# Kernel tuning notes

Measured on AMD Instinct MI355X. Metric: run time of the kernel, lower is better.

The kernel has to match this reference:

```python
import jax, jax.numpy as jnp
import numpy as np

DIM = 384
HEADS = 12
HEAD_DIM = DIM // HEADS
WS = 7          # window_size
SS = 3          # shift_size (SW-MSA)
DIM_FF = 4 * DIM
EPS = 1e-5


def _rel_pos_index():
    coords = np.stack(np.meshgrid(np.arange(WS), np.arange(WS), indexing='ij'))
    cf = coords.reshape(2, -1)                       # (2, 49)
    rel = cf[:, :, None] - cf[:, None, :]            # (2, 49, 49)
    rel = rel.transpose(1, 2, 0).astype(np.int64)
    rel[:, :, 0] += WS - 1
    rel[:, :, 1] += WS - 1
    rel[:, :, 0] *= 2 * WS - 1
    return rel.sum(-1)                               # (49, 49)


def _attn_mask(Hp, Wp):
    # cyclic-shift mask, computed on static shapes with numpy
    img = np.zeros((Hp, Wp))
    slices = (slice(0, -WS), slice(-WS, -SS), slice(-SS, None))
    cnt = 0
    for hs in slices:
        for ws_ in slices:
            img[hs, ws_] = cnt
            cnt += 1
    mw = img.reshape(Hp // WS, WS, Wp // WS, WS).transpose(0, 2, 1, 3).reshape(-1, WS * WS)
    am = mw[:, None, :] - mw[:, :, None]             # unsqueeze(1) - unsqueeze(2)
    am = np.where(am != 0, -100.0, 0.0)
    return jnp.asarray(am, jnp.float32)              # (nW, 49, 49)


def _ln(x, g, b):
    mu = jnp.mean(x, -1, keepdims=True)
    var = jnp.mean(jnp.square(x - mu), -1, keepdims=True)
    return (x - mu) * jax.lax.rsqrt(var + EPS) * g + b


def setup_inputs() -> dict:
    key = jax.random.key(0)
    ks = jax.random.split(key, 8)
    B, H, W = 32, 56, 56
    s = 0.02
    return {
        'x': jax.random.normal(ks[0], (B, H * W, DIM), jnp.float32),
        'H': H, 'W': W,
        'rel_idx': jnp.asarray(_rel_pos_index(), jnp.int32),
        'rpb_table': jax.random.normal(ks[1], ((2 * WS - 1) ** 2, HEADS), jnp.float32) * s,
        'qkv_w': jax.random.normal(ks[2], (DIM, 3 * DIM), jnp.float32) * s,
        'proj_w': jax.random.normal(ks[3], (DIM, DIM), jnp.float32) * s,
        'proj_b': jnp.zeros((DIM,), jnp.float32),
        'norm1_g': jnp.ones((DIM,), jnp.float32),
        'norm1_b': jnp.zeros((DIM,), jnp.float32),
        'norm2_g': jnp.ones((DIM,), jnp.float32),
        'norm2_b': jnp.zeros((DIM,), jnp.float32),
        'ffn_w1': jax.random.normal(ks[4], (DIM, DIM_FF), jnp.float32) * s,
        'ffn_b1': jnp.zeros((DIM_FF,), jnp.float32),
        'ffn_w2': jax.random.normal(ks[5], (DIM_FF, DIM), jnp.float32) * s,
        'ffn_b2': jnp.zeros((DIM,), jnp.float32),
    }


def reference(x, H, W, rel_idx, rpb_table, qkv_w, proj_w, proj_b,
              norm1_g, norm1_b, norm2_g, norm2_b,
              ffn_w1, ffn_b1, ffn_w2, ffn_b2):
    B, L, C = x.shape
    shortcut = x
    h = _ln(x, norm1_g, norm1_b).reshape(B, H, W, C)

    pad_b = (WS - H % WS) % WS
    pad_r = (WS - W % WS) % WS
    if pad_b > 0 or pad_r > 0:
        h = jnp.pad(h, ((0, 0), (0, pad_b), (0, pad_r), (0, 0)))
    Hp, Wp = H + pad_b, W + pad_r

    if SS > 0:
        h = jnp.roll(h, (-SS, -SS), axis=(1, 2))

    # window partition -> (B*nW, 49, C)
    nHw, nWw = Hp // WS, Wp // WS
    win = h.reshape(B, nHw, WS, nWw, WS, C).transpose(0, 1, 3, 2, 4, 5)
    win = win.reshape(-1, WS * WS, C)
    Bw, N = win.shape[0], WS * WS

    # window attention
    qkv = (win @ qkv_w).reshape(Bw, N, 3, HEADS, HEAD_DIM)
    q, k, v = [qkv[:, :, i].transpose(0, 2, 1, 3) for i in range(3)]  # (Bw, heads, N, hd)
    attn = jnp.einsum('bhnd,bhmd->bhnm', q, k) / np.sqrt(HEAD_DIM)

    bias = rpb_table[rel_idx]                      # (N, N, heads)
    attn = attn + bias.transpose(2, 0, 1)[None]

    if SS > 0:
        mask = _attn_mask(Hp, Wp)                  # (nW, N, N)
        nW = mask.shape[0]
        attn = attn.reshape(B, nW, HEADS, N, N) + mask[None, :, None]
        attn = attn.reshape(Bw, HEADS, N, N)

    attn = jax.nn.softmax(attn, axis=-1)
    out = jnp.einsum('bhnm,bhmd->bnhd', attn, v).reshape(Bw, N, C)
    out = out @ proj_w + proj_b

    # window reverse
    out = out.reshape(B, nHw, nWw, WS, WS, C).transpose(0, 1, 3, 2, 4, 5)
    out = out.reshape(B, Hp, Wp, C)
    if SS > 0:
        out = jnp.roll(out, (SS, SS), axis=(1, 2))
    if pad_b > 0 or pad_r > 0:
        out = out[:, :H, :W, :]

    h = shortcut + out.reshape(B, H * W, C)
    ff = _ln(h, norm2_g, norm2_b)
    ff = jax.nn.gelu(ff @ ffn_w1 + ffn_b1, approximate=False) @ ffn_w2 + ffn_b2
    return h + ff
```

## Files before the change

### kernel.cpp

```cpp
#include <hip/hip_runtime.h>

#define DEV __device__ __forceinline__

typedef __bf16 bf16x8 __attribute__((ext_vector_type(8)));
typedef float  f32x4  __attribute__((ext_vector_type(4)));
typedef unsigned short u16x8 __attribute__((ext_vector_type(8)));
typedef unsigned short u16x4 __attribute__((ext_vector_type(4)));
typedef long  longx2 __attribute__((ext_vector_type(2)));

DEV float b2f(unsigned short u) {
    unsigned int t = ((unsigned int)u) << 16;
    return __uint_as_float(t);
}
DEV unsigned short f2b(float f) {
    unsigned int u = __float_as_uint(f);
    unsigned int r = (u + 0x7FFFu + ((u >> 16) & 1u)) >> 16;
    return (unsigned short)r;
}
DEV unsigned char f2f8(float f) {
    return (unsigned char)(__builtin_amdgcn_cvt_pk_fp8_f32(f, f, 0, false) & 0xff);
}

DEV int kpos(int c) {
    int s = (c >> 3) & 7;
    return (c & ~63) | ((((s & 3) << 1) | (s >> 2)) << 3) | (c & 7);
}

DEV void gload_lds16(const void* g, void* l) {
    __builtin_amdgcn_global_load_lds(
        (const __attribute__((address_space(1))) void*)g,
        (__attribute__((address_space(3))) void*)l, 16, 0, 0);
}

DEV size_t win_to_tok(int row) {
    int w = row / 49, t = row - w * 49;
    int b  = w >> 6, widx = w & 63;
    int wi = widx >> 3, wj = widx & 7;
    int ti = t / 7, tj = t - ti * 7;
    int hh = wi * 7 + ti + 3; if (hh >= 56) hh -= 56;
    int ww = wj * 7 + tj + 3; if (ww >= 56) ww -= 56;
    return (size_t)b * 3136 + (size_t)hh * 56 + ww;
}

__global__ void wprep8(const float* __restrict__ src, unsigned char* __restrict__ dst,
                       int K, int N) {
    int idx = blockIdx.x * 256 + threadIdx.x;
    if (idx >= K * N) return;
    int k = idx / N, n = idx - k * N;
    dst[(size_t)n * K + kpos(k)] = f2f8(src[idx]);
}

__global__ void btab_build(const int* __restrict__ rel_idx, const float* __restrict__ rpb,
                           float* __restrict__ tab) {
    int idx = blockIdx.x * 256 + threadIdx.x;
    if (idx >= 4 * 12 * 64 * 64) return;
    int col = idx & 63, row = (idx >> 6) & 63;
    int h = (idx >> 12) % 12, cls = idx / (12 * 4096);
    float v;
    if (row >= 49 || col >= 49) {
        v = -10000.f;
    } else {
        v = rpb[rel_idx[row * 49 + col] * 12 + h];
        int ti = row / 7, tj = row - (row / 7) * 7;
        int si = col / 7, sj = col - (col / 7) * 7;
        int lq = ((cls & 2) ? (ti < 4 ? 1 : 2) : 0) * 3 + ((cls & 1) ? (tj < 4 ? 1 : 2) : 0);
        int lk = ((cls & 2) ? (si < 4 ? 1 : 2) : 0) * 3 + ((cls & 1) ? (sj < 4 ? 1 : 2) : 0);
        if (lq != lk) v -= 100.f;
    }
    tab[idx] = v;
}

template <int REMAP>
__global__ __launch_bounds__(256) void ln_kernel(const float* __restrict__ x,
                                                 const float* __restrict__ g,
                                                 const float* __restrict__ b,
                                                 unsigned char* __restrict__ out,
                                                 int rows) {
    int r = blockIdx.x * 4 + (threadIdx.x >> 6);
    int lane = threadIdx.x & 63;
    if (r >= rows) return;
    size_t src = REMAP ? win_to_tok(r) : (size_t)r;
    const float* xp = x + src * 384;
    float v[6];
    float s = 0.f;
#pragma unroll
    for (int i = 0; i < 6; ++i) { v[i] = xp[i * 64 + lane]; s += v[i]; }
#pragma unroll
    for (int off = 32; off; off >>= 1) s += __shfl_xor(s, off, 64);
    float mu = s * (1.f / 384.f);
    float q = 0.f;
#pragma unroll
    for (int i = 0; i < 6; ++i) { float d = v[i] - mu; q += d * d; }
#pragma unroll
    for (int off = 32; off; off >>= 1) q += __shfl_xor(q, off, 64);
    float inv = rsqrtf(q * (1.f / 384.f) + 1e-5f);
    unsigned char* op = out + (size_t)r * 384;
#pragma unroll
    for (int i = 0; i < 6; ++i) {
        int c = i * 64 + lane;
        op[kpos(c)] = f2f8((v[i] - mu) * inv * g[c] + b[c]);
    }
}

template <int MODE, int NBUF, int DEPTH, int SB, int MINW>
__global__ __launch_bounds__(256, MINW) void gemm_f8_kernel(const unsigned char* __restrict__ A,
                                                            const unsigned char* __restrict__ Bt,
                                                            int M, int N, int K,
                                                            const float* __restrict__ bias,
                                                            const float* __restrict__ resid,
                                                            unsigned char* __restrict__ outb8,
                                                            unsigned short* __restrict__ outb,
                                                            float* __restrict__ outf) {
    static_assert(SB ? (NBUF >= DEPTH + 2) : (NBUF >= DEPTH + 1), "ring too small");
    __shared__ unsigned char As[NBUF][128 * 64];
    __shared__ unsigned char Bs[NBUF][128 * 64];
    const int tid = threadIdx.x;
    const int wid = tid >> 6, lane = tid & 63;
    const int ntile = N >> 7;

    int bid = blockIdx.x;
    int nwg = gridDim.x;
    int swb = ((nwg & 7) == 0) ? ((bid & 7) * (nwg >> 3) + (bid >> 3)) : bid;
    const int mt = swb / ntile, nt = swb - mt * ntile;
    const int wr = wid >> 1, wc = wid & 1;

    f32x4 acc[4][4] = {};

    const unsigned char* Abase = A  + (size_t)(mt * 128) * K;
    const unsigned char* Bbase = Bt + (size_t)(nt * 128) * K;

    auto stage = [&](int buf, int k0) {
#pragma unroll
        for (int j = 0; j < 2; ++j) {
            int r  = j * 64 + (tid >> 2);
            int gp = (tid & 3) ^ ((r >> 1) & 3);
            gload_lds16(Abase + (size_t)r * K + k0 + gp * 16, &As[buf][j * 4096 + tid * 16]);
            gload_lds16(Bbase + (size_t)r * K + k0 + gp * 16, &Bs[buf][j * 4096 + tid * 16]);
        }
    };

    const int fr = lane & 15, kq = lane >> 4;
    const int rowA = wr * 64 + fr;
    const int rowB = wc * 64 + fr;
    const int cb = (kq ^ ((fr >> 1) & 3)) << 4;

    const int nk = K >> 6;
    stage(0, 0);
    if (DEPTH >= 2 && nk > 1) stage(1, 64);

    for (int t = 0; t < nk; ++t) {
        const int cur = t % NBUF;
        if (t + DEPTH < nk) {
            stage((t + DEPTH) % NBUF, (t + DEPTH) << 6);
            if constexpr (DEPTH == 1) {
                asm volatile("s_waitcnt vmcnt(4)" ::: "memory");
            } else {
                asm volatile("s_waitcnt vmcnt(8)" ::: "memory");
            }
        } else if (DEPTH >= 2 && t + 1 < nk) {
            asm volatile("s_waitcnt vmcnt(4)" ::: "memory");
        } else {
            asm volatile("s_waitcnt vmcnt(0)" ::: "memory");
        }
        __builtin_amdgcn_s_barrier();

        longx2 a[4], b[4];
#pragma unroll
        for (int m = 0; m < 4; ++m)
            a[m] = *(const longx2*)(&As[cur][(rowA + m * 16) * 64 + cb]);
#pragma unroll
        for (int n = 0; n < 4; ++n)
            b[n] = *(const longx2*)(&Bs[cur][(rowB + n * 16) * 64 + cb]);
#pragma unroll
        for (int ks = 0; ks < 2; ++ks)
#pragma unroll
            for (int m = 0; m < 4; ++m)
#pragma unroll
                for (int n = 0; n < 4; ++n)
                    acc[m][n] = __builtin_amdgcn_mfma_f32_16x16x32_fp8_fp8(b[n][ks], a[m][ks], acc[m][n], 0, 0, 0);

        asm volatile("s_waitcnt lgkmcnt(0)" ::: "memory");
        if constexpr (SB == 0) __builtin_amdgcn_s_barrier();
    }

    const int row0 = mt * 128 + wr * 64;
    const int col0 = nt * 128 + wc * 64;
    const int rl = lane & 15;
    const int cq = (lane >> 4) << 2;
#pragma unroll
    for (int m = 0; m < 4; ++m) {
        int row = row0 + m * 16 + rl;
        size_t tok = 0;
        if constexpr (MODE == 1) tok = win_to_tok(row);
#pragma unroll
        for (int n = 0; n < 4; ++n) {
            int col = col0 + n * 16 + cq;
            f32x4 v = acc[m][n];
            if constexpr (MODE == 0) {
                u16x4 pk;
#pragma unroll
                for (int r = 0; r < 4; ++r) pk[r] = f2b(v[r]);
                *(u16x4*)&outb[(size_t)row * N + col] = pk;
            } else if constexpr (MODE == 1) {
                size_t o = tok * 384 + col;
                f32x4 rv = *(const f32x4*)&resid[o];
                f32x4 bb = *(const f32x4*)&bias[col];
                f32x4 ov = rv + v + bb;
                *(f32x4*)&outf[o] = ov;
            } else if constexpr (MODE == 2) {
                f32x4 bb = *(const f32x4*)&bias[col];
                float g4[4];
#pragma unroll
                for (int r = 0; r < 4; ++r) {
                    float t2 = v[r] + bb[r];
                    g4[r] = t2 / (1.f + __expf(-1.702f * t2));
                }
                int pk = 0;
                pk = __builtin_amdgcn_cvt_pk_fp8_f32(g4[0], g4[1], pk, false);
                pk = __builtin_amdgcn_cvt_pk_fp8_f32(g4[2], g4[3], pk, true);
                *(int*)(outb8 + (size_t)row * N + kpos(col)) = pk;
            } else {
                size_t o = (size_t)row * N + col;
                f32x4 rv = *(const f32x4*)&resid[o];
                f32x4 bb = *(const f32x4*)&bias[col];
                f32x4 ov = rv + v + bb;
                *(f32x4*)&outf[o] = ov;
            }
        }
    }
}

__global__ __launch_bounds__(256, 2) void attn_kernel(const unsigned short* __restrict__ QKV,
                                                      const float* __restrict__ Btab,
                                                      unsigned char* __restrict__ O8) {
    __shared__ char lds[65536];
    char* Kl = lds;
    char* Vl = lds + 16384;
    char* Pl = lds + 32768;

    const int w   = blockIdx.x;
    const int tid = threadIdx.x, wid = tid >> 6, lane = tid & 63;
    const int fr  = lane & 15, kq = lane >> 4;
    const size_t base = (size_t)w * 49 * 1152;
    const int widx = w & 63, wi = widx >> 3, wj = widx & 7;
    const int cls = ((wi == 7) ? 2 : 0) | ((wj == 7) ? 1 : 0);
    const float* tb = Btab + (size_t)cls * 12 * 4096;
    constexpr float SCL = 0.17677669529663687f;

    for (int R = 0; R < 3; ++R) {
        if (R) __syncthreads();
        {
            f32x4 z = {};
#pragma unroll
            for (int j = 0; j < 8; ++j) *(f32x4*)(lds + j * 4096 + tid * 16) = z;
        }
        __syncthreads();
        {
            int hh = tid >> 6, h = R * 4 + hh;
#pragma unroll
            for (int it = 0; it < 4; ++it) {
                int i = (tid & 63) + it * 64;
                if (i < 196) {
                    int m = i >> 2, c = i & 3;
                    u16x8 kv = *(const u16x8*)&QKV[base + (size_t)m * 1152 + 384 + h * 32 + c * 8];
                    *(u16x8*)(Kl + hh * 4096 + m * 64 + (c ^ ((m >> 1) & 3)) * 16) = kv;
                    u16x8 vv = *(const u16x8*)&QKV[base + (size_t)m * 1152 + 768 + h * 32 + c * 8];
#pragma unroll
                    for (int j = 0; j < 8; ++j) {
                        int d = c * 8 + j;
                        *(unsigned short*)(Vl + hh * 4096 + d * 128 +
                                           (((m >> 3) ^ (d & 7)) * 16) + (m & 7) * 2) = vv[j];
                    }
                }
            }
        }
        __syncthreads();

        const int h = R * 4 + wid;
        const float* tbh = tb + h * 4096;

        bf16x8 aq[4], bk[4];
#pragma unroll
        for (int mi = 0; mi < 4; ++mi) {
            int row = mi * 16 + fr; if (row > 48) row = 48;
            aq[mi] = *(const bf16x8*)&QKV[base + (size_t)row * 1152 + h * 32 + kq * 8];
        }
#pragma unroll
        for (int ni = 0; ni < 4; ++ni) {
            int rk = ni * 16 + fr;
            bk[ni] = *(const bf16x8*)(Kl + wid * 4096 + rk * 64 + ((kq ^ ((rk >> 1) & 3)) * 16));
        }
        f32x4 s[4][4] = {};
#pragma unroll
        for (int mi = 0; mi < 4; ++mi)
#pragma unroll
            for (int ni = 0; ni < 4; ++ni)
                s[mi][ni] = __builtin_amdgcn_mfma_f32_16x16x32_bf16(bk[ni], aq[mi], s[mi][ni], 0, 0, 0);

        float linv_[4];
#pragma unroll
        for (int mi = 0; mi < 4; ++mi) {
            int row = mi * 16 + fr;
            const float* tr = tbh + row * 64 + kq * 4;
            f32x4 sv[4];
            float mx = -1e30f;
#pragma unroll
            for (int ni = 0; ni < 4; ++ni) {
                f32x4 bb = *(const f32x4*)&tr[ni * 16];
                sv[ni] = s[mi][ni] * SCL + bb;
                mx = fmaxf(mx, fmaxf(fmaxf(sv[ni][0], sv[ni][1]), fmaxf(sv[ni][2], sv[ni][3])));
            }
            mx = fmaxf(mx, __shfl_xor(mx, 16, 64));
            mx = fmaxf(mx, __shfl_xor(mx, 32, 64));
            float sm = 0.f;
#pragma unroll
            for (int ni = 0; ni < 4; ++ni)
#pragma unroll
                for (int r = 0; r < 4; ++r) { sv[ni][r] = __expf(sv[ni][r] - mx); sm += sv[ni][r]; }
            sm += __shfl_xor(sm, 16, 64);
            sm += __shfl_xor(sm, 32, 64);
            linv_[mi] = 1.f / sm;
#pragma unroll
            for (int ni = 0; ni < 4; ++ni) {
                int colb = ni * 16 + kq * 4;
                int phys = (colb >> 3) ^ (row & 7);
                u16x4 pk;
#pragma unroll
                for (int r = 0; r < 4; ++r) pk[r] = f2b(sv[ni][r]);
                *(u16x4*)(Pl + wid * 8192 + row * 128 + phys * 16 + (colb & 7) * 2) = pk;
            }
        }
        asm volatile("s_waitcnt lgkmcnt(0)" ::: "memory");
        __builtin_amdgcn_sched_barrier(0);

        f32x4 oacc[4][2] = {};
#pragma unroll
        for (int sl = 0; sl < 2; ++sl) {
            bf16x8 bv[2];
#pragma unroll
            for (int ni = 0; ni < 2; ++ni) {
                int d = ni * 16 + fr;
                bv[ni] = *(const bf16x8*)(Vl + wid * 4096 + d * 128 + (((sl * 4 + kq) ^ (d & 7)) * 16));
            }
#pragma unroll
            for (int mi = 0; mi < 4; ++mi) {
                int row = mi * 16 + fr;
                bf16x8 ap = *(const bf16x8*)(Pl + wid * 8192 + row * 128 + (((sl * 4 + kq) ^ (row & 7)) * 16));
#pragma unroll
                for (int ni = 0; ni < 2; ++ni)
                    oacc[mi][ni] = __builtin_amdgcn_mfma_f32_16x16x32_bf16(bv[ni], ap, oacc[mi][ni], 0, 0, 0);
            }
        }

#pragma unroll
        for (int mi = 0; mi < 4; ++mi) {
            int row = mi * 16 + fr;
            if (row < 49) {
                float li = linv_[mi];
                unsigned char* opb = O8 + (size_t)(w * 49 + row) * 384;
#pragma unroll
                for (int ni = 0; ni < 2; ++ni) {
                    int c = h * 32 + ni * 16 + kq * 4;
                    int pk = 0;
                    pk = __builtin_amdgcn_cvt_pk_fp8_f32(oacc[mi][ni][0] * li, oacc[mi][ni][1] * li, pk, false);
                    pk = __builtin_amdgcn_cvt_pk_fp8_f32(oacc[mi][ni][2] * li, oacc[mi][ni][3] * li, pk, true);
                    *(int*)(opb + kpos(c)) = pk;
                }
            }
        }
    }
}

extern "C" void kernel_launch(void* const* d_in, const int* in_sizes, int n_in,
                              void* d_out, int out_size, void* d_ws, size_t ws_size,
                              hipStream_t stream) {
    const float* x     = (const float*)d_in[0];
    const int*   rel   = (const int*)  d_in[3];
    const float* rpb   = (const float*)d_in[4];
    const float* qkvw  = (const float*)d_in[5];
    const float* projw = (const float*)d_in[6];
    const float* projb = (const float*)d_in[7];
    const float* n1g   = (const float*)d_in[8];
    const float* n1b   = (const float*)d_in[9];
    const float* n2g   = (const float*)d_in[10];
    const float* n2b   = (const float*)d_in[11];
    const float* w1    = (const float*)d_in[12];
    const float* b1    = (const float*)d_in[13];
    const float* w2    = (const float*)d_in[14];
    const float* b2    = (const float*)d_in[15];
    float* out = (float*)d_out;

    const int T = in_sizes[0] / 384;

    char* ws = (char*)d_ws;
    size_t off = 0;
    auto alloc = [&](size_t bytes) {
        char* p = ws + off;
        off += (bytes + 255) & ~(size_t)255;
        return p;
    };
    unsigned char* Wq8  = (unsigned char*)alloc((size_t)1152 * 384);
    unsigned char* Wp8  = (unsigned char*)alloc((size_t)384 * 384);
    unsigned char* W18  = (unsigned char*)alloc((size_t)1536 * 384);
    unsigned char* W28  = (unsigned char*)alloc((size_t)384 * 1536);
    float*         Btab = (float*)       alloc((size_t)4 * 12 * 4096 * 4);
    unsigned char* slotA = (unsigned char*)alloc((size_t)T * 384);
    unsigned char* slotB = (unsigned char*)alloc((size_t)T * 1152 * 2);

    unsigned char*  X1  = slotA;
    unsigned char*  O8  = slotA;
    unsigned char*  X2  = slotA;
    unsigned short* QKV = (unsigned short*)slotB;
    unsigned char*  F8  = slotB;
    float*          Hh  = out;

    wprep8<<<dim3((1152 * 384 + 255) / 256), 256, 0, stream>>>(qkvw, Wq8, 384, 1152);
    wprep8<<<dim3((384 * 384 + 255) / 256),  256, 0, stream>>>(projw, Wp8, 384, 384);
    wprep8<<<dim3((384 * 1536 + 255) / 256), 256, 0, stream>>>(w1, W18, 384, 1536);
    wprep8<<<dim3((1536 * 384 + 255) / 256), 256, 0, stream>>>(w2, W28, 1536, 384);
    btab_build<<<dim3((4 * 12 * 4096 + 255) / 256), 256, 0, stream>>>(rel, rpb, Btab);

    ln_kernel<1><<<dim3(T / 4), 256, 0, stream>>>(x, n1g, n1b, X1, T);
    gemm_f8_kernel<0, 2, 1, 0, 4><<<dim3((T / 128) * (1152 / 128)), 256, 0, stream>>>(
        X1, Wq8, T, 1152, 384, nullptr, nullptr, nullptr, QKV, nullptr);
    attn_kernel<<<dim3(T / 49), 256, 0, stream>>>(QKV, Btab, O8);
    gemm_f8_kernel<1, 2, 1, 0, 4><<<dim3((T / 128) * (384 / 128)), 256, 0, stream>>>(
        O8, Wp8, T, 384, 384, projb, x, nullptr, nullptr, Hh);
    ln_kernel<0><<<dim3(T / 4), 256, 0, stream>>>(Hh, n2g, n2b, X2, T);
    gemm_f8_kernel<2, 2, 1, 0, 4><<<dim3((T / 128) * (1536 / 128)), 256, 0, stream>>>(
        X2, W18, T, 1536, 384, b1, nullptr, F8, nullptr, nullptr);
    gemm_f8_kernel<3, 4, 2, 1, 2><<<dim3((T / 128) * (384 / 128)), 256, 0, stream>>>(
        F8, W28, T, 384, 1536, b2, Hh, nullptr, nullptr, out);
}
```

Before: 678.9 us.

## Store QKV in fp8 and run QK^T attention MFMA in fp8

The QKV GEMM now writes fp8 instead of bf16, which halves the QKV intermediate traffic. The attention kernel loads fp8 Q and K straight into fp8 MFMAs and converts V from fp8 to bf16 when staging it in LDS, so the LDS footprint shrinks. The window-to-token index mapping for the projection epilogue is precomputed into a table, and two divisions are replaced by hardware reciprocals. The price is lower precision for Q, K and V, plus an extra small kernel launch.

```diff
diff --git a/kernel.cpp b/kernel.cpp
--- a/kernel.cpp
+++ b/kernel.cpp
@@ -40,6 +40,11 @@
     int hh = wi * 7 + ti + 3; if (hh >= 56) hh -= 56;
     int ww = wj * 7 + tj + 3; if (ww >= 56) ww -= 56;
     return (size_t)b * 3136 + (size_t)hh * 56 + ww;
+}
+
+__global__ void tokmap_build(int* __restrict__ tm, int T) {
+    int i = blockIdx.x * 256 + threadIdx.x;
+    if (i < T) tm[i] = (int)win_to_tok(i);
 }
 
 __global__ void wprep8(const float* __restrict__ src, unsigned char* __restrict__ dst,
@@ -108,8 +113,8 @@
                                                             int M, int N, int K,
                                                             const float* __restrict__ bias,
                                                             const float* __restrict__ resid,
+                                                            const int* __restrict__ tokmap,
                                                             unsigned char* __restrict__ outb8,
-                                                            unsigned short* __restrict__ outb,
                                                             float* __restrict__ outf) {
     static_assert(SB ? (NBUF >= DEPTH + 2) : (NBUF >= DEPTH + 1), "ring too small");
     __shared__ unsigned char As[NBUF][128 * 64];
@@ -191,16 +196,16 @@
     for (int m = 0; m < 4; ++m) {
         int row = row0 + m * 16 + rl;
         size_t tok = 0;
-        if constexpr (MODE == 1) tok = win_to_tok(row);
+        if constexpr (MODE == 1) tok = (size_t)tokmap[row];
 #pragma unroll
         for (int n = 0; n < 4; ++n) {
             int col = col0 + n * 16 + cq;
             f32x4 v = acc[m][n];
             if constexpr (MODE == 0) {
-                u16x4 pk;
-#pragma unroll
-                for (int r = 0; r < 4; ++r) pk[r] = f2b(v[r]);
-                *(u16x4*)&outb[(size_t)row * N + col] = pk;
+                int pk = 0;
+                pk = __builtin_amdgcn_cvt_pk_fp8_f32(v[0], v[1], pk, false);
+                pk = __builtin_amdgcn_cvt_pk_fp8_f32(v[2], v[3], pk, true);
+                *(int*)(outb8 + (size_t)row * N + col) = pk;
             } else if constexpr (MODE == 1) {
                 size_t o = tok * 384 + col;
                 f32x4 rv = *(const f32x4*)&resid[o];
@@ -213,7 +218,8 @@
 #pragma unroll
                 for (int r = 0; r < 4; ++r) {
                     float t2 = v[r] + bb[r];
-                    g4[r] = t2 / (1.f + __expf(-1.702f * t2));
+                    float e  = __expf(-1.702f * t2);
+                    g4[r] = t2 * __builtin_amdgcn_rcpf(1.f + e);
                 }
                 int pk = 0;
                 pk = __builtin_amdgcn_cvt_pk_fp8_f32(g4[0], g4[1], pk, false);
@@ -230,13 +236,13 @@
     }
 }
 
-__global__ __launch_bounds__(256, 2) void attn_kernel(const unsigned short* __restrict__ QKV,
+__global__ __launch_bounds__(256, 2) void attn_kernel(const unsigned char* __restrict__ QKV8,
                                                       const float* __restrict__ Btab,
                                                       unsigned char* __restrict__ O8) {
-    __shared__ char lds[65536];
+    __shared__ char lds[8192 + 16384 + 32768];
     char* Kl = lds;
-    char* Vl = lds + 16384;
-    char* Pl = lds + 32768;
+    char* Vl = lds + 8192;
+    char* Pl = lds + 24576;
 
     const int w   = blockIdx.x;
     const int tid = threadIdx.x, wid = tid >> 6, lane = tid & 63;
@@ -252,7 +258,7 @@
         {
             f32x4 z = {};
 #pragma unroll
-            for (int j = 0; j < 8; ++j) *(f32x4*)(lds + j * 4096 + tid * 16) = z;
+            for (int j = 0; j < 6; ++j) *(f32x4*)(lds + j * 4096 + tid * 16) = z;
         }
         __syncthreads();
         {
@@ -262,14 +268,25 @@
                 int i = (tid & 63) + it * 64;
                 if (i < 196) {
                     int m = i >> 2, c = i & 3;
-                    u16x8 kv = *(const u16x8*)&QKV[base + (size_t)m * 1152 + 384 + h * 32 + c * 8];
-                    *(u16x8*)(Kl + hh * 4096 + m * 64 + (c ^ ((m >> 1) & 3)) * 16) = kv;
-                    u16x8 vv = *(const u16x8*)&QKV[base + (size_t)m * 1152 + 768 + h * 32 + c * 8];
+                    long k8 = *(const long*)(QKV8 + base + (size_t)m * 1152 + 384 + h * 32 + c * 8);
+                    int s = c ^ (m & 3) ^ ((m >> 2) & 3);
+                    *(long*)(Kl + hh * 2048 + m * 32 + s * 8) = k8;
+                    long v8 = *(const long*)(QKV8 + base + (size_t)m * 1152 + 768 + h * 32 + c * 8);
+                    int lo = (int)v8, hi = (int)(v8 >> 32);
+                    float vf[8];
+                    vf[0] = __builtin_amdgcn_cvt_f32_fp8(lo, 0);
+                    vf[1] = __builtin_amdgcn_cvt_f32_fp8(lo, 1);
+                    vf[2] = __builtin_amdgcn_cvt_f32_fp8(lo, 2);
+                    vf[3] = __builtin_amdgcn_cvt_f32_fp8(lo, 3);
+                    vf[4] = __builtin_amdgcn_cvt_f32_fp8(hi, 0);
+                    vf[5] = __builtin_amdgcn_cvt_f32_fp8(hi, 1);
+                    vf[6] = __builtin_amdgcn_cvt_f32_fp8(hi, 2);
+                    vf[7] = __builtin_amdgcn_cvt_f32_fp8(hi, 3);
 #pragma unroll
                     for (int j = 0; j < 8; ++j) {
                         int d = c * 8 + j;
                         *(unsigned short*)(Vl + hh * 4096 + d * 128 +
-                                           (((m >> 3) ^ (d & 7)) * 16) + (m & 7) * 2) = vv[j];
+                                           (((m >> 3) ^ (d & 7)) * 16) + (m & 7) * 2) = f2b(vf[j]);
                     }
                 }
             }
@@ -279,23 +296,24 @@
         const int h = R * 4 + wid;
         const float* tbh = tb + h * 4096;
 
-        bf16x8 aq[4], bk[4];
+        long aq[4], bk[4];
 #pragma unroll
         for (int mi = 0; mi < 4; ++mi) {
             int row = mi * 16 + fr; if (row > 48) row = 48;
-            aq[mi] = *(const bf16x8*)&QKV[base + (size_t)row * 1152 + h * 32 + kq * 8];
+            aq[mi] = *(const long*)(QKV8 + base + (size_t)row * 1152 + h * 32 + kq * 8);
         }
 #pragma unroll
         for (int ni = 0; ni < 4; ++ni) {
             int rk = ni * 16 + fr;
-            bk[ni] = *(const bf16x8*)(Kl + wid * 4096 + rk * 64 + ((kq ^ ((rk >> 1) & 3)) * 16));
+            bk[ni] = *(const long*)(Kl + wid * 2048 + rk * 32 +
+                                    ((kq ^ (rk & 3) ^ ((rk >> 2) & 3)) * 8));
         }
         f32x4 s[4][4] = {};
 #pragma unroll
         for (int mi = 0; mi < 4; ++mi)
 #pragma unroll
             for (int ni = 0; ni < 4; ++ni)
-                s[mi][ni] = __builtin_amdgcn_mfma_f32_16x16x32_bf16(bk[ni], aq[mi], s[mi][ni], 0, 0, 0);
+                s[mi][ni] = __builtin_amdgcn_mfma_f32_16x16x32_fp8_fp8(bk[ni], aq[mi], s[mi][ni], 0, 0, 0);
 
         float linv_[4];
 #pragma unroll
@@ -319,7 +337,7 @@
                 for (int r = 0; r < 4; ++r) { sv[ni][r] = __expf(sv[ni][r] - mx); sm += sv[ni][r]; }
             sm += __shfl_xor(sm, 16, 64);
             sm += __shfl_xor(sm, 32, 64);
-            linv_[mi] = 1.f / sm;
+            linv_[mi] = __builtin_amdgcn_rcpf(sm);
 #pragma unroll
             for (int ni = 0; ni < 4; ++ni) {
                 int colb = ni * 16 + kq * 4;
@@ -404,31 +422,33 @@
     unsigned char* W18  = (unsigned char*)alloc((size_t)1536 * 384);
     unsigned char* W28  = (unsigned char*)alloc((size_t)384 * 1536);
     float*         Btab = (float*)       alloc((size_t)4 * 12 * 4096 * 4);
+    int*           Tmap = (int*)         alloc((size_t)T * 4);
     unsigned char* slotA = (unsigned char*)alloc((size_t)T * 384);
-    unsigned char* slotB = (unsigned char*)alloc((size_t)T * 1152 * 2);
-
-    unsigned char*  X1  = slotA;
-    unsigned char*  O8  = slotA;
-    unsigned char*  X2  = slotA;
-    unsigned short* QKV = (unsigned short*)slotB;
-    unsigned char*  F8  = slotB;
-    float*          Hh  = out;
+    unsigned char* slotB = (unsigned char*)alloc((size_t)T * 1536);
+
+    unsigned char* X1   = slotA;
+    unsigned char* O8   = slotA;
+    unsigned char* X2   = slotA;
+    unsigned char* QKV8 = slotB;
+    unsigned char* F8   = slotB;
+    float*         Hh   = out;
 
     wprep8<<<dim3((1152 * 384 + 255) / 256), 256, 0, stream>>>(qkvw, Wq8, 384, 1152);
     wprep8<<<dim3((384 * 384 + 255) / 256),  256, 0, stream>>>(projw, Wp8, 384, 384);
     wprep8<<<dim3((384 * 1536 + 255) / 256), 256, 0, stream>>>(w1, W18, 384, 1536);
     wprep8<<<dim3((1536 * 384 + 255) / 256), 256, 0, stream>>>(w2, W28, 1536, 384);
     btab_build<<<dim3((4 * 12 * 4096 + 255) / 256), 256, 0, stream>>>(rel, rpb, Btab);
+    tokmap_build<<<dim3((T + 255) / 256), 256, 0, stream>>>(Tmap, T);
 
     ln_kernel<1><<<dim3(T / 4), 256, 0, stream>>>(x, n1g, n1b, X1, T);
     gemm_f8_kernel<0, 2, 1, 0, 4><<<dim3((T / 128) * (1152 / 128)), 256, 0, stream>>>(
-        X1, Wq8, T, 1152, 384, nullptr, nullptr, nullptr, QKV, nullptr);
-    attn_kernel<<<dim3(T / 49), 256, 0, stream>>>(QKV, Btab, O8);
+        X1, Wq8, T, 1152, 384, nullptr, nullptr, nullptr, QKV8, nullptr);
+    attn_kernel<<<dim3(T / 49), 256, 0, stream>>>(QKV8, Btab, O8);
     gemm_f8_kernel<1, 2, 1, 0, 4><<<dim3((T / 128) * (384 / 128)), 256, 0, stream>>>(
-        O8, Wp8, T, 384, 384, projb, x, nullptr, nullptr, Hh);
+        O8, Wp8, T, 384, 384, projb, x, Tmap, nullptr, Hh);
     ln_kernel<0><<<dim3(T / 4), 256, 0, stream>>>(Hh, n2g, n2b, X2, T);
     gemm_f8_kernel<2, 2, 1, 0, 4><<<dim3((T / 128) * (1536 / 128)), 256, 0, stream>>>(
-        X2, W18, T, 1536, 384, b1, nullptr, F8, nullptr, nullptr);
+        X2, W18, T, 1536, 384, b1, nullptr, nullptr, F8, nullptr);
     gemm_f8_kernel<3, 4, 2, 1, 2><<<dim3((T / 128) * (384 / 128)), 256, 0, stream>>>(
         F8, W28, T, 384, 1536, b2, Hh, nullptr, nullptr, out);
 }
```

Result: faster. 662.1 us (-2.5%).
